# Kernel optimization log

Measured on AMD Instinct MI355X. Metric: run time of the kernel, lower is better.

Reference implementation:

```python
import jax, jax.numpy as jnp
import numpy as np

HEADS = 8
DIM_HEAD = 64
QUERY_DIM = 1024
CONTEXT_DIM = 768
INNER = HEADS * DIM_HEAD  # 512


def setup_inputs() -> dict:
    key = jax.random.key(0)
    ks = jax.random.split(key, 7)
    B, Sq, Skv = 4, 4096, 1024
    x = jax.random.normal(ks[0], (B, Sq, QUERY_DIM), dtype=jnp.float32)
    context = jax.random.normal(ks[1], (B, Skv, CONTEXT_DIM), dtype=jnp.float32)
    # nn.Linear(in, out) weights stored as [out, in]; we use [in, out] for x @ W
    Wq = jax.random.normal(ks[2], (QUERY_DIM, INNER), dtype=jnp.float32) * (QUERY_DIM ** -0.5)
    Wk = jax.random.normal(ks[3], (CONTEXT_DIM, INNER), dtype=jnp.float32) * (CONTEXT_DIM ** -0.5)
    Wv = jax.random.normal(ks[4], (CONTEXT_DIM, INNER), dtype=jnp.float32) * (CONTEXT_DIM ** -0.5)
    Wo = jax.random.normal(ks[5], (INNER, QUERY_DIM), dtype=jnp.float32) * (INNER ** -0.5)
    bo = jax.random.normal(ks[6], (QUERY_DIM,), dtype=jnp.float32) * 0.01
    return {"x": x, "context": context, "Wq": Wq, "Wk": Wk, "Wv": Wv, "Wo": Wo, "bo": bo}


def reference(x, context, Wq, Wk, Wv, Wo, bo):
    B, Sq, _ = x.shape
    h, d = HEADS, DIM_HEAD
    scale = d ** -0.5
    # project and split heads: [B, S, h*d] -> [B, h, S, d]
    q = (x @ Wq).reshape(B, Sq, h, d).transpose(0, 2, 1, 3)
    k = (context @ Wk).reshape(B, -1, h, d).transpose(0, 2, 1, 3)
    v = (context @ Wv).reshape(B, -1, h, d).transpose(0, 2, 1, 3)
    # the torch chunked loop is exactly full softmax attention (softmax is row-wise)
    scores = jnp.einsum('bhid,bhjd->bhij', q, k) * scale
    attn = jax.nn.softmax(scores, axis=-1)
    out = jnp.einsum('bhij,bhjd->bhid', attn, v)  # [B, h, Sq, d]
    out = out.transpose(0, 2, 1, 3).reshape(B, Sq, h * d)
    return out @ Wo + bo
```

## Files before the change

### kernel.cpp

```cpp
#include <hip/hip_runtime.h>

#define SQ 4096
#define SKV 1024
#define BATCH 4
#define NH 8
#define DH 64
#define QD 1024
#define CD 768
#define INNER 512

typedef _Float16 half8 __attribute__((ext_vector_type(8)));
typedef _Float16 half4v __attribute__((ext_vector_type(4)));
typedef float floatx4 __attribute__((ext_vector_type(4)));
typedef unsigned int uint4v __attribute__((ext_vector_type(4)));

#define MFMA16(a, b, c) __builtin_amdgcn_mfma_f32_16x16x32_f16(a, b, c, 0, 0, 0)

#define GLD16(gptr, lptr)                                                            \
  __builtin_amdgcn_global_load_lds(                                                  \
      (const __attribute__((address_space(1))) unsigned int*)(const void*)(gptr),    \
      (__attribute__((address_space(3))) unsigned int*)(void*)(lptr), 16, 0, 0)

__global__ __launch_bounds__(256) void transpose_all(const float* __restrict__ Wq,
                                                     const float* __restrict__ Wk,
                                                     const float* __restrict__ Wv,
                                                     const float* __restrict__ Wo,
                                                     _Float16* __restrict__ wqt,
                                                     _Float16* __restrict__ wkvt,
                                                     _Float16* __restrict__ wot) {
  __shared__ float tile[32][33];
  const int z = blockIdx.z;
  const float* src; _Float16* dst; int R, C;
  if (z == 0)      { src = Wq; dst = wqt;                        R = QD;    C = INNER; }
  else if (z == 1) { src = Wk; dst = wkvt;                       R = CD;    C = INNER; }
  else if (z == 2) { src = Wv; dst = wkvt + (size_t)INNER * CD;  R = CD;    C = INNER; }
  else             { src = Wo; dst = wot;                        R = INNER; C = QD;   }
  const int c0 = blockIdx.x * 32, r0 = blockIdx.y * 32;
  if (c0 >= C || r0 >= R) return;
  const int tx = threadIdx.x & 31, ty = threadIdx.x >> 5;
#pragma unroll
  for (int i = 0; i < 32; i += 8)
    tile[ty + i][tx] = src[(size_t)(r0 + ty + i) * C + c0 + tx];
  __syncthreads();
#pragma unroll
  for (int i = 0; i < 32; i += 8)
    dst[(size_t)(c0 + ty + i) * R + r0 + tx] = (_Float16)tile[tx][ty + i];
}

template <int MODE, int AF32>
__global__ __launch_bounds__(256) void gemm128(const void* __restrict__ Aany,
                                               const _Float16* __restrict__ Bt,
                                               void* __restrict__ Cout,
                                               void* __restrict__ Cout2,
                                               const float* __restrict__ bias,
                                               int M, int N, int K) {
  __shared__ char AsRaw[AF32 ? 128 * 32 * 4 : 128 * 32 * 2];
  __shared__ _Float16 Bs[128 * 32];
  float* As32 = (float*)AsRaw;
  _Float16* As16 = (_Float16*)AsRaw;

  const int tid = threadIdx.x;
  const int wave = tid >> 6, lane = tid & 63;
  const int quad = lane >> 4, l16 = lane & 15;
  const int wm = (wave >> 1) * 64, wn = (wave & 1) * 64;
  const size_t n0 = (size_t)blockIdx.x * 128, m0 = (size_t)blockIdx.y * 128;

  floatx4 acc[4][4] = {};

  const float* a32g = (const float*)Aany + (m0 + (tid >> 3)) * (size_t)K + (tid & 7) * 4;
  const _Float16* a16g = (const _Float16*)Aany + (m0 + (tid >> 2)) * (size_t)K + (tid & 3) * 8;
  const _Float16* bg = Bt + (n0 + (tid >> 2)) * (size_t)K + (tid & 3) * 8;

  for (int k0 = 0; k0 < K; k0 += 32) {
    __syncthreads();
    if (AF32) {
#pragma unroll
      for (int j = 0; j < 4; ++j)
        GLD16(a32g + k0 + (size_t)j * 32 * K, As32 + tid * 4 + j * 1024);
    } else {
#pragma unroll
      for (int j = 0; j < 2; ++j)
        GLD16(a16g + k0 + (size_t)j * 64 * K, As16 + tid * 8 + j * 2048);
    }
#pragma unroll
    for (int j = 0; j < 2; ++j)
      GLD16(bg + k0 + (size_t)j * 64 * K, Bs + tid * 8 + j * 2048);
    __syncthreads();

    half8 af[4], bf[4];
#pragma unroll
    for (int mt = 0; mt < 4; ++mt) {
      const int row = wm + mt * 16 + l16;
      if (AF32) {
        floatx4 x0 = *(const floatx4*)(As32 + row * 32 + quad * 8);
        floatx4 x1 = *(const floatx4*)(As32 + row * 32 + quad * 8 + 4);
        half8 t;
#pragma unroll
        for (int i = 0; i < 4; ++i) { t[i] = (_Float16)x0[i]; t[4 + i] = (_Float16)x1[i]; }
        af[mt] = t;
      } else {
        af[mt] = *(const half8*)(As16 + row * 32 + quad * 8);
      }
    }
#pragma unroll
    for (int nt = 0; nt < 4; ++nt)
      bf[nt] = *(const half8*)(Bs + (wn + nt * 16 + l16) * 32 + quad * 8);
#pragma unroll
    for (int mt = 0; mt < 4; ++mt)
#pragma unroll
      for (int nt = 0; nt < 4; ++nt)
        acc[mt][nt] = MFMA16(af[mt], bf[nt], acc[mt][nt]);
  }

  if (MODE == 0 || MODE == 3) {
    _Float16* C = (_Float16*)Cout;
    const float sc = (MODE == 3) ? 0.125f * 1.44269504088896f : 1.0f;
#pragma unroll
    for (int mt = 0; mt < 4; ++mt) {
      const size_t row = m0 + wm + mt * 16 + quad * 4;
#pragma unroll
      for (int nt = 0; nt < 4; ++nt) {
        const size_t col = n0 + wn + nt * 16 + l16;
#pragma unroll
        for (int r = 0; r < 4; ++r)
          C[(row + r) * N + col] = (_Float16)(acc[mt][nt][r] * sc);
      }
    }
  } else if (MODE == 4) {
    if (n0 < INNER) {
      _Float16* C = (_Float16*)Cout;
#pragma unroll
      for (int mt = 0; mt < 4; ++mt) {
        const size_t row = m0 + wm + mt * 16 + quad * 4;
#pragma unroll
        for (int nt = 0; nt < 4; ++nt) {
          const size_t col = n0 + wn + nt * 16 + l16;
#pragma unroll
          for (int r = 0; r < 4; ++r)
            C[(row + r) * INNER + col] = (_Float16)acc[mt][nt][r];
        }
      }
    } else {
      _Float16* C = (_Float16*)Cout2;
      const int b = (int)(m0 >> 10);
#pragma unroll
      for (int mt = 0; mt < 4; ++mt) {
        const int kvb = (int)(m0 & 1023) + wm + mt * 16 + quad * 4;
#pragma unroll
        for (int nt = 0; nt < 4; ++nt) {
          const int col = (int)(n0 - INNER + wn + nt * 16 + l16);
          const int h = col >> 6, d = col & 63;
          half4v pk;
#pragma unroll
          for (int r = 0; r < 4; ++r) pk[r] = (_Float16)acc[mt][nt][r];
          *(half4v*)(C + (size_t)((b * NH + h) * DH + d) * SKV + kvb) = pk;
        }
      }
    }
  } else {
    float* C = (float*)Cout;
#pragma unroll
    for (int mt = 0; mt < 4; ++mt) {
      const size_t row = m0 + wm + mt * 16 + quad * 4;
#pragma unroll
      for (int nt = 0; nt < 4; ++nt) {
        const size_t col = n0 + wn + nt * 16 + l16;
        const float bb = bias[col];
#pragma unroll
        for (int r = 0; r < 4; ++r)
          C[(row + r) * N + col] = acc[mt][nt][r] + bb;
      }
    }
  }
}

__global__ __launch_bounds__(256, 3) void flash_attn6(const _Float16* __restrict__ Q,
                                                      const _Float16* __restrict__ Kp,
                                                      const _Float16* __restrict__ Vt,
                                                      _Float16* __restrict__ O) {
  __shared__ _Float16 Ks[128 * 64];
  __shared__ _Float16 Vs[64 * 128];
  const int tid = threadIdx.x;
  const int wave = tid >> 6, lane = tid & 63;
  const int quad = lane >> 4, l16 = lane & 15;
  const int x7 = l16 & 7;

  const int flat = blockIdx.x;
  const int nf = (flat & 7) * 128 + (flat >> 3);
  const int qblk = nf & 31, bh = nf >> 5;
  const int b = bh >> 3, h = bh & 7;

  const size_t qrow0 = (size_t)b * SQ + qblk * 128 + wave * 32;
  const _Float16* qptr = Q + qrow0 * INNER + h * DH;
  const _Float16* kbase = Kp + (size_t)b * SKV * INNER + h * DH;
  const _Float16* vbase = Vt + (size_t)bh * DH * SKV;

  const int kr = tid >> 3;
  const int kb = (tid & 7) ^ (kr & 7);
  const _Float16* kg = kbase + (size_t)kr * INNER + kb * 8;
  _Float16* kl = Ks + tid * 8;
  const int vr = tid >> 4;
  const int vsb = (tid & 8) | ((tid & 7) ^ (vr & 7));
  const _Float16* vg = vbase + (size_t)vr * SKV + vsb * 8;
  _Float16* vl = Vs + tid * 8;

  half8 aq[2][2];
#pragma unroll
  for (int hh = 0; hh < 2; ++hh) {
    aq[hh][0] = *(const half8*)(qptr + (size_t)(hh * 16 + l16) * INNER + quad * 8);
    aq[hh][1] = *(const half8*)(qptr + (size_t)(hh * 16 + l16) * INNER + 32 + quad * 8);
  }

  floatx4 o[2][4] = {};
  float lsum[2] = {0.f, 0.f};

  const int koffA = (quad ^ x7) << 3;
  const int koffB = ((quad + 4) ^ x7) << 3;

  for (int t = 0; t < SKV / 128; ++t) {
    __syncthreads();
#pragma unroll
    for (int i = 0; i < 4; ++i)
      GLD16(kg + (size_t)(t * 128 + i * 32) * INNER, kl + i * 2048);
#pragma unroll
    for (int i = 0; i < 4; ++i)
      GLD16(vg + (size_t)(i * 16) * SKV + t * 128, vl + i * 2048);
    __syncthreads();

#pragma unroll
    for (int c = 0; c < 4; ++c) {
      const _Float16* kbA = Ks + (c * 32 + l16) * 64;
      half8 k0a = *(const half8*)(kbA + koffA);
      half8 k0b = *(const half8*)(kbA + koffB);
      half8 k1a = *(const half8*)(kbA + 16 * 64 + koffA);
      half8 k1b = *(const half8*)(kbA + 16 * 64 + koffB);

      half8 ap2[2];
#pragma unroll
      for (int hh = 0; hh < 2; ++hh) {
        floatx4 st0 = {0.f, 0.f, 0.f, 0.f}, st1 = {0.f, 0.f, 0.f, 0.f};
        st0 = MFMA16(k0a, aq[hh][0], st0);
        st0 = MFMA16(k0b, aq[hh][1], st0);
        st1 = MFMA16(k1a, aq[hh][0], st1);
        st1 = MFMA16(k1b, aq[hh][1], st1);

        float p0[4], p1[4];
#pragma unroll
        for (int r = 0; r < 4; ++r) {
          p0[r] = __builtin_exp2f(st0[r]);
          p1[r] = __builtin_exp2f(st1[r]);
        }
        lsum[hh] += (p0[0] + p0[1] + p0[2] + p0[3]) + (p1[0] + p1[1] + p1[2] + p1[3]);

        unsigned pk00 = __builtin_bit_cast(unsigned, __builtin_amdgcn_cvt_pkrtz(p0[0], p0[1]));
        unsigned pk01 = __builtin_bit_cast(unsigned, __builtin_amdgcn_cvt_pkrtz(p0[2], p0[3]));
        unsigned pk10 = __builtin_bit_cast(unsigned, __builtin_amdgcn_cvt_pkrtz(p1[0], p1[1]));
        unsigned pk11 = __builtin_bit_cast(unsigned, __builtin_amdgcn_cvt_pkrtz(p1[2], p1[3]));

        const int bsel = ((lane & 16) << 1) + l16;
        const bool jlo = (lane & 32) == 0;
        unsigned s00 = __shfl(pk00, bsel);
        unsigned s10 = __shfl(pk10, bsel);
        unsigned s01 = __shfl(pk01, bsel);
        unsigned s11 = __shfl(pk11, bsel);
        unsigned s00b = __shfl(pk00, bsel + 16);
        unsigned s10b = __shfl(pk10, bsel + 16);
        unsigned s01b = __shfl(pk01, bsel + 16);
        unsigned s11b = __shfl(pk11, bsel + 16);
        uint4v wv;
        wv[0] = jlo ? s00 : s10;
        wv[1] = jlo ? s01 : s11;
        wv[2] = jlo ? s00b : s10b;
        wv[3] = jlo ? s01b : s11b;
        ap2[hh] = __builtin_bit_cast(half8, wv);
      }

      const int vb = c * 4 + quad;
      const int vblks = (vb & 8) | ((vb & 7) ^ x7);
#pragma unroll
      for (int nt = 0; nt < 4; ++nt) {
        half8 bv = *(const half8*)(Vs + (nt * 16 + l16) * 128 + vblks * 8);
        o[0][nt] = MFMA16(ap2[0], bv, o[0][nt]);
        o[1][nt] = MFMA16(ap2[1], bv, o[1][nt]);
      }
    }
  }

  float tot[2];
#pragma unroll
  for (int hh = 0; hh < 2; ++hh) {
    float v = lsum[hh];
    v += __shfl_xor(v, 16);
    v += __shfl_xor(v, 32);
    tot[hh] = v;
  }
  float inv[2][4];
#pragma unroll
  for (int hh = 0; hh < 2; ++hh)
#pragma unroll
    for (int r = 0; r < 4; ++r)
      inv[hh][r] = 1.0f / __shfl(tot[hh], quad * 4 + r);

  _Float16* op = O + qrow0 * INNER + h * DH;
#pragma unroll
  for (int hh = 0; hh < 2; ++hh)
#pragma unroll
    for (int nt = 0; nt < 4; ++nt)
#pragma unroll
      for (int r = 0; r < 4; ++r)
        op[(size_t)(hh * 16 + quad * 4 + r) * INNER + nt * 16 + l16] =
            (_Float16)(o[hh][nt][r] * inv[hh][r]);
}

extern "C" void kernel_launch(void* const* d_in, const int* in_sizes, int n_in,
                              void* d_out, int out_size, void* d_ws, size_t ws_size,
                              hipStream_t stream) {
  const float* x   = (const float*)d_in[0];
  const float* ctx = (const float*)d_in[1];
  const float* Wq  = (const float*)d_in[2];
  const float* Wk  = (const float*)d_in[3];
  const float* Wv  = (const float*)d_in[4];
  const float* Wo  = (const float*)d_in[5];
  const float* bo  = (const float*)d_in[6];
  float* out = (float*)d_out;

  _Float16* ws = (_Float16*)d_ws;
  _Float16* wqt  = ws;
  _Float16* wkvt = wqt + (size_t)INNER * QD;
  _Float16* wot  = wkvt + (size_t)2 * INNER * CD;
  _Float16* qh   = wot + (size_t)QD * INNER;
  _Float16* kh   = qh + (size_t)BATCH * SQ * INNER;
  _Float16* vth  = kh + (size_t)BATCH * SKV * INNER;
  _Float16* aoh  = vth + (size_t)BATCH * SKV * INNER;

  transpose_all<<<dim3(32, 32, 4), 256, 0, stream>>>(Wq, Wk, Wv, Wo, wqt, wkvt, wot);

  gemm128<3, 1><<<dim3(INNER / 128, BATCH * SQ / 128), 256, 0, stream>>>(
      (const void*)x, wqt, (void*)qh, nullptr, nullptr, BATCH * SQ, INNER, QD);
  gemm128<4, 1><<<dim3(2 * INNER / 128, BATCH * SKV / 128), 256, 0, stream>>>(
      (const void*)ctx, wkvt, (void*)kh, (void*)vth, nullptr, BATCH * SKV, 2 * INNER, CD);

  flash_attn6<<<dim3(BATCH * NH * SQ / 128), 256, 0, stream>>>(qh, kh, vth, aoh);

  gemm128<2, 0><<<dim3(QD / 128, BATCH * SQ / 128), 256, 0, stream>>>(
      (const void*)aoh, wot, (void*)out, nullptr, bo, BATCH * SQ, QD, INNER);
}
```

Measured before the change: 295.2 us.

## Rewrite flash attention with 32x32 MFMA, permlane swaps, and double-buffered KV

Rewrites the attention kernel to use 32x32x16 MFMA tiles. The P matrix is relaid out with v_permlane32_swap instead of eight shuffles per tile. The row sum is computed by an MFMA against a ones vector rather than scalar adds and cross-lane reductions. K/V tiles are double-buffered in 64-row chunks, so the global-to-LDS loads for the next tile overlap compute and one barrier per iteration is dropped. This adds MFMA work for the sum and more accumulator registers, which may hurt occupancy.

After: 288.1 us. -2.4%, faster.

```diff
diff --git a/kernel.cpp b/kernel.cpp
--- a/kernel.cpp
+++ b/kernel.cpp
@@ -12,9 +12,13 @@
 typedef _Float16 half8 __attribute__((ext_vector_type(8)));
 typedef _Float16 half4v __attribute__((ext_vector_type(4)));
 typedef float floatx4 __attribute__((ext_vector_type(4)));
+typedef float f32x16 __attribute__((ext_vector_type(16)));
 typedef unsigned int uint4v __attribute__((ext_vector_type(4)));
 
 #define MFMA16(a, b, c) __builtin_amdgcn_mfma_f32_16x16x32_f16(a, b, c, 0, 0, 0)
+#define MFMA32(a, b, c) __builtin_amdgcn_mfma_f32_32x32x16_f16(a, b, c, 0, 0, 0)
+
+#define PLSWAP(a, b) asm("v_permlane32_swap_b32 %0, %1" : "+v"(a), "+v"(b))
 
 #define GLD16(gptr, lptr)                                                            \
   __builtin_amdgcn_global_load_lds(                                                  \
@@ -174,16 +178,15 @@
   }
 }
 
-__global__ __launch_bounds__(256, 3) void flash_attn6(const _Float16* __restrict__ Q,
+__global__ __launch_bounds__(256, 3) void flash_attn7(const _Float16* __restrict__ Q,
                                                       const _Float16* __restrict__ Kp,
                                                       const _Float16* __restrict__ Vt,
                                                       _Float16* __restrict__ O) {
-  __shared__ _Float16 Ks[128 * 64];
-  __shared__ _Float16 Vs[64 * 128];
+  __shared__ _Float16 Ksb[2 * 64 * 64];
+  __shared__ _Float16 Vsb[2 * 64 * 64];
   const int tid = threadIdx.x;
   const int wave = tid >> 6, lane = tid & 63;
-  const int quad = lane >> 4, l16 = lane & 15;
-  const int x7 = l16 & 7;
+  const int l31 = lane & 31, hi = lane >> 5, x7 = lane & 7;
 
   const int flat = blockIdx.x;
   const int nf = (flat & 7) * 128 + (flat >> 3);
@@ -198,118 +201,100 @@
   const int kr = tid >> 3;
   const int kb = (tid & 7) ^ (kr & 7);
   const _Float16* kg = kbase + (size_t)kr * INNER + kb * 8;
-  _Float16* kl = Ks + tid * 8;
-  const int vr = tid >> 4;
-  const int vsb = (tid & 8) | ((tid & 7) ^ (vr & 7));
-  const _Float16* vg = vbase + (size_t)vr * SKV + vsb * 8;
-  _Float16* vl = Vs + tid * 8;
-
-  half8 aq[2][2];
-#pragma unroll
-  for (int hh = 0; hh < 2; ++hh) {
-    aq[hh][0] = *(const half8*)(qptr + (size_t)(hh * 16 + l16) * INNER + quad * 8);
-    aq[hh][1] = *(const half8*)(qptr + (size_t)(hh * 16 + l16) * INNER + 32 + quad * 8);
+  const _Float16* vg = vbase + (size_t)kr * SKV + kb * 8;
+
+#define STAGE_KV(bi, tt)                                                        \
+  do {                                                                          \
+    _Float16* _kl = Ksb + (bi) * 4096 + tid * 8;                                \
+    _Float16* _vl = Vsb + (bi) * 4096 + tid * 8;                                \
+    GLD16(kg + (size_t)((tt) * 64) * INNER, _kl);                               \
+    GLD16(kg + (size_t)((tt) * 64 + 32) * INNER, _kl + 2048);                   \
+    GLD16(vg + (tt) * 64, _vl);                                                 \
+    GLD16(vg + (size_t)32 * SKV + (tt) * 64, _vl + 2048);                       \
+  } while (0)
+
+  half8 aq[4];
+#pragma unroll
+  for (int i = 0; i < 4; ++i)
+    aq[i] = *(const half8*)(qptr + (size_t)l31 * INNER + i * 16 + hi * 8);
+
+  int koff[4], voffB[4];
+#pragma unroll
+  for (int i = 0; i < 4; ++i)
+    koff[i] = l31 * 64 + (((i * 2 + hi) ^ x7) << 3);
+#pragma unroll
+  for (int j = 0; j < 4; ++j)
+    voffB[j] = l31 * 64 + (((j * 2 + hi) ^ x7) << 3);
+
+  half8 ones;
+#pragma unroll
+  for (int j = 0; j < 8; ++j) ones[j] = (_Float16)1.0f;
+
+  f32x16 o0 = {}, o1 = {}, osum = {};
+
+  STAGE_KV(0, 0);
+
+  for (int t = 0; t < SKV / 64; ++t) {
+    __syncthreads();
+    if (t < SKV / 64 - 1) STAGE_KV((t + 1) & 1, t + 1);
+    const _Float16* ks = Ksb + (t & 1) * 4096;
+    const _Float16* vs = Vsb + (t & 1) * 4096;
+
+#pragma unroll
+    for (int c2 = 0; c2 < 2; ++c2) {
+      half8 ak[4];
+#pragma unroll
+      for (int i = 0; i < 4; ++i)
+        ak[i] = *(const half8*)(ks + c2 * 2048 + koff[i]);
+
+      f32x16 st = {};
+#pragma unroll
+      for (int i = 0; i < 4; ++i) st = MFMA32(ak[i], aq[i], st);
+
+      unsigned w[8];
+#pragma unroll
+      for (int j = 0; j < 8; ++j) {
+        float plo = __builtin_exp2f(st[2 * j]);
+        float phi = __builtin_exp2f(st[2 * j + 1]);
+        w[j] = __builtin_bit_cast(unsigned, __builtin_amdgcn_cvt_pkrtz(plo, phi));
+      }
+      PLSWAP(w[0], w[2]);
+      PLSWAP(w[1], w[3]);
+      PLSWAP(w[4], w[6]);
+      PLSWAP(w[5], w[7]);
+      uint4v u0 = {w[0], w[1], w[2], w[3]};
+      uint4v u1 = {w[4], w[5], w[6], w[7]};
+      half8 A0 = __builtin_bit_cast(half8, u0);
+      half8 A1 = __builtin_bit_cast(half8, u1);
+
+      osum = MFMA32(A0, ones, osum);
+      osum = MFMA32(A1, ones, osum);
+
+      {
+        half8 bv00 = *(const half8*)(vs + 0 * 2048 + voffB[c2 * 2 + 0]);
+        half8 bv10 = *(const half8*)(vs + 1 * 2048 + voffB[c2 * 2 + 0]);
+        o0 = MFMA32(A0, bv00, o0);
+        o1 = MFMA32(A0, bv10, o1);
+        half8 bv01 = *(const half8*)(vs + 0 * 2048 + voffB[c2 * 2 + 1]);
+        half8 bv11 = *(const half8*)(vs + 1 * 2048 + voffB[c2 * 2 + 1]);
+        o0 = MFMA32(A1, bv01, o0);
+        o1 = MFMA32(A1, bv11, o1);
+      }
+    }
   }
 
-  floatx4 o[2][4] = {};
-  float lsum[2] = {0.f, 0.f};
-
-  const int koffA = (quad ^ x7) << 3;
-  const int koffB = ((quad + 4) ^ x7) << 3;
-
-  for (int t = 0; t < SKV / 128; ++t) {
-    __syncthreads();
-#pragma unroll
-    for (int i = 0; i < 4; ++i)
-      GLD16(kg + (size_t)(t * 128 + i * 32) * INNER, kl + i * 2048);
-#pragma unroll
-    for (int i = 0; i < 4; ++i)
-      GLD16(vg + (size_t)(i * 16) * SKV + t * 128, vl + i * 2048);
-    __syncthreads();
-
-#pragma unroll
-    for (int c = 0; c < 4; ++c) {
-      const _Float16* kbA = Ks + (c * 32 + l16) * 64;
-      half8 k0a = *(const half8*)(kbA + koffA);
-      half8 k0b = *(const half8*)(kbA + koffB);
-      half8 k1a = *(const half8*)(kbA + 16 * 64 + koffA);
-      half8 k1b = *(const half8*)(kbA + 16 * 64 + koffB);
-
-      half8 ap2[2];
-#pragma unroll
-      for (int hh = 0; hh < 2; ++hh) {
-        floatx4 st0 = {0.f, 0.f, 0.f, 0.f}, st1 = {0.f, 0.f, 0.f, 0.f};
-        st0 = MFMA16(k0a, aq[hh][0], st0);
-        st0 = MFMA16(k0b, aq[hh][1], st0);
-        st1 = MFMA16(k1a, aq[hh][0], st1);
-        st1 = MFMA16(k1b, aq[hh][1], st1);
-
-        float p0[4], p1[4];
-#pragma unroll
-        for (int r = 0; r < 4; ++r) {
-          p0[r] = __builtin_exp2f(st0[r]);
-          p1[r] = __builtin_exp2f(st1[r]);
-        }
-        lsum[hh] += (p0[0] + p0[1] + p0[2] + p0[3]) + (p1[0] + p1[1] + p1[2] + p1[3]);
-
-        unsigned pk00 = __builtin_bit_cast(unsigned, __builtin_amdgcn_cvt_pkrtz(p0[0], p0[1]));
-        unsigned pk01 = __builtin_bit_cast(unsigned, __builtin_amdgcn_cvt_pkrtz(p0[2], p0[3]));
-        unsigned pk10 = __builtin_bit_cast(unsigned, __builtin_amdgcn_cvt_pkrtz(p1[0], p1[1]));
-        unsigned pk11 = __builtin_bit_cast(unsigned, __builtin_amdgcn_cvt_pkrtz(p1[2], p1[3]));
-
-        const int bsel = ((lane & 16) << 1) + l16;
-        const bool jlo = (lane & 32) == 0;
-        unsigned s00 = __shfl(pk00, bsel);
-        unsigned s10 = __shfl(pk10, bsel);
-        unsigned s01 = __shfl(pk01, bsel);
-        unsigned s11 = __shfl(pk11, bsel);
-        unsigned s00b = __shfl(pk00, bsel + 16);
-        unsigned s10b = __shfl(pk10, bsel + 16);
-        unsigned s01b = __shfl(pk01, bsel + 16);
-        unsigned s11b = __shfl(pk11, bsel + 16);
-        uint4v wv;
-        wv[0] = jlo ? s00 : s10;
-        wv[1] = jlo ? s01 : s11;
-        wv[2] = jlo ? s00b : s10b;
-        wv[3] = jlo ? s01b : s11b;
-        ap2[hh] = __builtin_bit_cast(half8, wv);
-      }
-
-      const int vb = c * 4 + quad;
-      const int vblks = (vb & 8) | ((vb & 7) ^ x7);
-#pragma unroll
-      for (int nt = 0; nt < 4; ++nt) {
-        half8 bv = *(const half8*)(Vs + (nt * 16 + l16) * 128 + vblks * 8);
-        o[0][nt] = MFMA16(ap2[0], bv, o[0][nt]);
-        o[1][nt] = MFMA16(ap2[1], bv, o[1][nt]);
-      }
-    }
+  float inv16[16];
+#pragma unroll
+  for (int r = 0; r < 16; ++r) inv16[r] = 1.0f / osum[r];
+
+  _Float16* op = O + qrow0 * INNER + h * DH;
+#pragma unroll
+  for (int r = 0; r < 16; ++r) {
+    const int q = (r & 3) + 8 * (r >> 2) + 4 * hi;
+    op[(size_t)q * INNER + l31] = (_Float16)(o0[r] * inv16[r]);
+    op[(size_t)q * INNER + 32 + l31] = (_Float16)(o1[r] * inv16[r]);
   }
-
-  float tot[2];
-#pragma unroll
-  for (int hh = 0; hh < 2; ++hh) {
-    float v = lsum[hh];
-    v += __shfl_xor(v, 16);
-    v += __shfl_xor(v, 32);
-    tot[hh] = v;
-  }
-  float inv[2][4];
-#pragma unroll
-  for (int hh = 0; hh < 2; ++hh)
-#pragma unroll
-    for (int r = 0; r < 4; ++r)
-      inv[hh][r] = 1.0f / __shfl(tot[hh], quad * 4 + r);
-
-  _Float16* op = O + qrow0 * INNER + h * DH;
-#pragma unroll
-  for (int hh = 0; hh < 2; ++hh)
-#pragma unroll
-    for (int nt = 0; nt < 4; ++nt)
-#pragma unroll
-      for (int r = 0; r < 4; ++r)
-        op[(size_t)(hh * 16 + quad * 4 + r) * INNER + nt * 16 + l16] =
-            (_Float16)(o[hh][nt][r] * inv[hh][r]);
+#undef STAGE_KV
 }
 
 extern "C" void kernel_launch(void* const* d_in, const int* in_sizes, int n_in,
@@ -340,7 +325,7 @@
   gemm128<4, 1><<<dim3(2 * INNER / 128, BATCH * SKV / 128), 256, 0, stream>>>(
       (const void*)ctx, wkvt, (void*)kh, (void*)vth, nullptr, BATCH * SKV, 2 * INNER, CD);
 
-  flash_attn6<<<dim3(BATCH * NH * SQ / 128), 256, 0, stream>>>(qh, kh, vth, aoh);
+  flash_attn7<<<dim3(BATCH * NH * SQ / 128), 256, 0, stream>>>(qh, kh, vth, aoh);
 
   gemm128<2, 0><<<dim3(QD / 128, BATCH * SQ / 128), 256, 0, stream>>>(
       (const void*)aoh, wot, (void*)out, nullptr, bo, BATCH * SQ, QD, INNER);
```
